# Kernel optimization log

Hardware: AMD Instinct MI355X
Metric: run time of the kernel (lower is better)

## Reference

```python
import jax, jax.numpy as jnp
import numpy as np

B, N, IN_DIM = 4, 2048, 128
HID, OUT_DIM, HEADS = 64, 64, 4
NEG = -1e9


def setup_inputs() -> dict:
    key = jax.random.key(0)
    ks = jax.random.split(key, 6)
    x = jax.random.normal(ks[0], (B, N, IN_DIM), dtype=jnp.float32)
    adj_matrix = jax.random.randint(ks[1], (B, N, N), 0, 2, dtype=jnp.int32)
    # per-head params: W [H, IN, HID], a [H, 2*HID] (Linear(2*HID,1) weight)
    W_heads = jax.random.normal(ks[2], (HEADS, IN_DIM, HID), dtype=jnp.float32) / np.sqrt(IN_DIM)
    a_heads = jax.random.normal(ks[3], (HEADS, 2 * HID), dtype=jnp.float32) / np.sqrt(2 * HID)
    W_out = jax.random.normal(ks[4], (HEADS * HID, OUT_DIM), dtype=jnp.float32) / np.sqrt(HEADS * HID)
    a_out = jax.random.normal(ks[5], (2 * OUT_DIM,), dtype=jnp.float32) / np.sqrt(2 * OUT_DIM)
    return {"x": x, "adj_matrix": adj_matrix, "W_heads": W_heads,
            "a_heads": a_heads, "W_out": W_out, "a_out": a_out}


def gat_layer(x, W, a, adj):
    # h: [B, N, D]
    h = jnp.einsum('bni,id->bnd', x, W)
    d = h.shape[-1]
    # a . [h_i ; h_j] = h_i . a1 + h_j . a2  (avoids N^2 concat materialization)
    s = h @ a[:d]          # [B, N] source term
    t = h @ a[d:]          # [B, N] target term
    e = s[:, :, None] + t[:, None, :]              # [B, N, N]
    e = jax.nn.leaky_relu(e, negative_slope=0.2)
    e = jnp.where(adj == 0, jnp.float32(NEG), e)
    alpha = jax.nn.softmax(e, axis=-1)             # dropout is identity in eval
    return jnp.einsum('bij,bjd->bid', alpha, h)


def reference(x, adj_matrix, W_heads, a_heads, W_out, a_out):
    # multi-head: vmap over head-stacked params -> [H, B, N, HID]
    heads = jax.vmap(gat_layer, in_axes=(None, 0, 0, None))(x, W_heads, a_heads, adj_matrix)
    # concat heads along feature dim: [B, N, H*HID]
    hcat = jnp.transpose(heads, (1, 2, 0, 3)).reshape(x.shape[0], x.shape[1], -1)
    return gat_layer(hcat, W_out, a_out, adj_matrix)
```

## Files before the change

kernel.cpp:

```cpp
#include <hip/hip_runtime.h>

#define B_ 4
#define N_ 2048
#define IND_ 128
#define NH_ 4

typedef short short8 __attribute__((ext_vector_type(8)));
typedef float float4v __attribute__((ext_vector_type(4)));

#if __has_builtin(__builtin_amdgcn_sbfe)
#define SBFE(x, o) __builtin_amdgcn_sbfe((int)(x), (unsigned)(o), 1u)
#else
#define SBFE(x, o) (((int)((unsigned)(x) << (31 - (o)))) >> 31)
#endif

typedef __attribute__((address_space(1))) const unsigned int as1_u32;
typedef __attribute__((address_space(3))) unsigned int as3_u32;
__device__ __forceinline__ void gl_lds16(const void* g, void* l) {
  __builtin_amdgcn_global_load_lds((as1_u32*)g, (as3_u32*)l, 16, 0, 0);
}

__device__ __forceinline__ unsigned int f2b_bits(float f) {
  unsigned int u = __float_as_uint(f);
  u += 0x7fffu + ((u >> 16) & 1u);
  return u >> 16;
}
__device__ __forceinline__ unsigned int pack_rne(float lo, float hi) {
  return f2b_bits(lo) | (f2b_bits(hi) << 16);
}
__device__ __forceinline__ unsigned int pack_trunc(float lo, float hi) {
  return __builtin_amdgcn_perm(__float_as_uint(hi), __float_as_uint(lo), 0x07060302u);
}
__device__ __forceinline__ float trunc_bf(float f) {
  return __uint_as_float(__float_as_uint(f) & 0xFFFF0000u);
}

union u4s8 { uint4 u; short8 s; };

__global__ __launch_bounds__(256) void gat_k0(
    const int* __restrict__ adj, unsigned long long* __restrict__ adjm,
    const float* __restrict__ Wh, const float* __restrict__ ah,
    const float* __restrict__ Wo, const float* __restrict__ ao,
    uint4* __restrict__ Wpk1, uint4* __restrict__ Wpk3,
    float* __restrict__ vsp1, float* __restrict__ vsp3) {
  const int bid = blockIdx.x;
  const int t = threadIdx.x;
  if (bid < B_ * N_ * N_ / 256) {
    const int gid = bid * 256 + t;
    const unsigned long long mval = __ballot(adj[gid] != 0);
    if ((t & 63) == 0) adjm[gid >> 6] = mval;
    return;
  }
  const int pb = bid - B_ * N_ * N_ / 256;
  if (pb < 32) {
    const int id = pb * 256 + t, e = id >> 6, l = id & 63;
    const int p = e & 1, ks = (e >> 1) & 3, dt = (e >> 3) & 3, h = e >> 5;
    const int d = dt * 16 + (l & 15), kb = ks * 32 + (l >> 4) * 8;
    unsigned u[4];
#pragma unroll
    for (int i = 0; i < 4; i++) {
      float w0 = Wh[(size_t)(h * IND_ + kb + 2 * i) * 64 + d];
      float w1 = Wh[(size_t)(h * IND_ + kb + 2 * i + 1) * 64 + d];
      if (p) {
        w0 -= __uint_as_float(f2b_bits(w0) << 16);
        w1 -= __uint_as_float(f2b_bits(w1) << 16);
      }
      u[i] = pack_rne(w0, w1);
    }
    Wpk1[e * 64 + l] = make_uint4(u[0], u[1], u[2], u[3]);
  } else if (pb < 48) {
    const int id = (pb - 32) * 256 + t, e = id >> 6, l = id & 63;
    const int p = e & 1, ks = (e >> 1) & 7, dt = e >> 4;
    const int d = dt * 16 + (l & 15), kb = ks * 32 + (l >> 4) * 8;
    unsigned u[4];
#pragma unroll
    for (int i = 0; i < 4; i++) {
      float w0 = Wo[(size_t)(kb + 2 * i) * 64 + d];
      float w1 = Wo[(size_t)(kb + 2 * i + 1) * 64 + d];
      if (p) {
        w0 -= __uint_as_float(f2b_bits(w0) << 16);
        w1 -= __uint_as_float(f2b_bits(w1) << 16);
      }
      u[i] = pack_rne(w0, w1);
    }
    Wpk3[e * 64 + l] = make_uint4(u[0], u[1], u[2], u[3]);
  } else if (pb < 52) {
    const int id = (pb - 48) * 256 + t;
    const int h = id >> 8, vec = (id >> 7) & 1, k = id & 127;
    const float* wr = Wh + (size_t)(h * IND_ + k) * 64;
    const float* av = ah + h * 128 + vec * 64;
    float s = 0.f;
#pragma unroll 8
    for (int d = 0; d < 64; d++) s = fmaf(wr[d], av[d], s);
    vsp1[(h * 2 + vec) * 128 + k] = s;
  } else {
    const int id = (pb - 52) * 256 + t;
    const int vec = id >> 8, k = id & 255;
    const float* wr = Wo + (size_t)k * 64;
    const float* av = ao + vec * 64;
    float s = 0.f;
#pragma unroll 8
    for (int d = 0; d < 64; d++) s = fmaf(wr[d], av[d], s);
    vsp3[vec * 256 + k] = s;
  }
}

__global__ __launch_bounds__(256) void gat_k1(
    const float* __restrict__ x, const uint4* __restrict__ Wpk1,
    const float* __restrict__ vsp1,
    unsigned short* __restrict__ h1T, float2* __restrict__ Es1, float2* __restrict__ Et1) {
  __shared__ float xf[16 * 132];
  __shared__ unsigned short xhi[16 * 136];
  __shared__ unsigned short xlo[16 * 136];
  const int b = blockIdx.y, j0 = blockIdx.x * 16;
  const int tid = threadIdx.x;
  const int jr = tid >> 4, k0 = (tid & 15) * 8;
  const float4* xg = (const float4*)(x + ((size_t)b * N_ + j0 + jr) * IND_ + k0);
  const float4 v0 = xg[0], v1 = xg[1];
  *(float4*)(xf + jr * 132 + k0) = v0;
  *(float4*)(xf + jr * 132 + k0 + 4) = v1;
  {
    unsigned hu[4], lu[4];
    hu[0] = pack_trunc(v0.x, v0.y); hu[1] = pack_trunc(v0.z, v0.w);
    hu[2] = pack_trunc(v1.x, v1.y); hu[3] = pack_trunc(v1.z, v1.w);
    lu[0] = pack_trunc(v0.x - trunc_bf(v0.x), v0.y - trunc_bf(v0.y));
    lu[1] = pack_trunc(v0.z - trunc_bf(v0.z), v0.w - trunc_bf(v0.w));
    lu[2] = pack_trunc(v1.x - trunc_bf(v1.x), v1.y - trunc_bf(v1.y));
    lu[3] = pack_trunc(v1.z - trunc_bf(v1.z), v1.w - trunc_bf(v1.w));
    *(uint4*)(xhi + jr * 136 + k0) = make_uint4(hu[0], hu[1], hu[2], hu[3]);
    *(uint4*)(xlo + jr * 136 + k0) = make_uint4(lu[0], lu[1], lu[2], lu[3]);
  }
  __syncthreads();
  const int h = tid >> 6, lane = tid & 63;
  const int m = lane & 15, q = lane >> 4;
  float4v acc[4] = {};
  const unsigned short* ap = xhi + m * 136 + q * 8;
  const unsigned short* alp = xlo + m * 136 + q * 8;
#pragma unroll
  for (int ks = 0; ks < 4; ks++) {
    const short8 ahi = *(const short8*)(ap + ks * 32);
    const short8 alo = *(const short8*)(alp + ks * 32);
#pragma unroll
    for (int dt = 0; dt < 4; dt++) {
      u4s8 bh, bl;
      bh.u = Wpk1[(((h * 4 + dt) * 4 + ks) * 2 + 0) * 64 + lane];
      bl.u = Wpk1[(((h * 4 + dt) * 4 + ks) * 2 + 1) * 64 + lane];
      acc[dt] = __builtin_amdgcn_mfma_f32_16x16x32_bf16(ahi, bh.s, acc[dt], 0, 0, 0);
      acc[dt] = __builtin_amdgcn_mfma_f32_16x16x32_bf16(alo, bh.s, acc[dt], 0, 0, 0);
      acc[dt] = __builtin_amdgcn_mfma_f32_16x16x32_bf16(ahi, bl.s, acc[dt], 0, 0, 0);
    }
  }
  const int hb = b * NH_ + h;
#pragma unroll
  for (int dt = 0; dt < 4; dt++) {
    const uint2 uu = make_uint2(pack_rne(acc[dt][0], acc[dt][1]),
                                pack_rne(acc[dt][2], acc[dt][3]));
    *(uint2*)(h1T + (size_t)(hb * 64 + dt * 16 + m) * N_ + j0 + q * 4) = uu;
  }
  const int vec = (tid >> 5) & 1, jd = (tid >> 1) & 15, half = tid & 1;
  const float* xr = xf + jd * 132 + half * 64;
  const float* vr = vsp1 + (h * 2 + vec) * 128 + half * 64;
  float dot = 0.f;
#pragma unroll
  for (int kk = 0; kk < 64; kk += 4) {
    const float4 xa = *(const float4*)(xr + kk);
    const float4 va = *(const float4*)(vr + kk);
    dot = fmaf(xa.x, va.x, dot); dot = fmaf(xa.y, va.y, dot);
    dot = fmaf(xa.z, va.z, dot); dot = fmaf(xa.w, va.w, dot);
  }
  dot += __shfl_xor(dot, 1);
  if (half == 0) {
    const float2 ev = make_float2(__expf(dot), __expf(0.2f * dot));
    if (vec == 0) Es1[(size_t)hb * N_ + j0 + jd] = ev;
    else          Et1[(size_t)hb * N_ + j0 + jd] = ev;
  }
}

__global__ __launch_bounds__(256) void gat_k2(
    const unsigned char* __restrict__ adjm, const unsigned short* __restrict__ h1T,
    const float2* __restrict__ Es1, const float2* __restrict__ Et1,
    float* __restrict__ hcat) {
  __shared__ float4 Ebuf[1024];
  __shared__ uint4 vbuf[2][256];
  const int b = blockIdx.z, h = blockIdx.y;
  const int tid = threadIdx.x;
  const int wv = tid >> 6, lane = tid & 63;
  const int m = lane & 15, q = lane >> 4;
  const int i0 = blockIdx.x * 64 + wv * 16;
  const int hb = b * NH_ + h;
  {
    const char* esrc = (const char*)(Et1 + (size_t)hb * N_);
    char* edst = (char*)Ebuf;
#pragma unroll
    for (int c = 0; c < 4; c++)
      gl_lds16(esrc + c * 4096 + tid * 16, edst + c * 4096 + tid * 16);
  }
  const char* vsrc = (const char*)(h1T + ((size_t)hb * 64 + (tid >> 2)) * N_) + (tid & 3) * 16;
  gl_lds16(vsrc, (char*)vbuf[0] + tid * 16);
  const float2 G = Es1[(size_t)hb * N_ + i0 + m];
  const float G1 = G.x, G2 = G.y;
  const float NSE = 1.0f / G1;
  const unsigned char* mrow = adjm + (size_t)(b * N_ + i0 + m) * (N_ / 8);
  const int q8 = q * 8;
  float4v acc[4] = {};
  float4v accS = {};
  const short8 ONES = {0x3F80, 0x3F80, 0x3F80, 0x3F80, 0x3F80, 0x3F80, 0x3F80, 0x3F80};
  uint4 mw = *(const uint4*)mrow;
  for (int it4 = 0; it4 < 16; it4++) {
#pragma unroll
    for (int s = 0; s < 4; s++) {
      const int it = it4 * 4 + s;
      __syncthreads();
      if (it + 1 < 64) gl_lds16(vsrc + (it + 1) * 64, (char*)vbuf[(it + 1) & 1] + tid * 16);
      const unsigned mword = s == 0 ? mw.x : s == 1 ? mw.y : s == 2 ? mw.z : mw.w;
      if (s == 3 && it4 < 15) mw = *(const uint4*)(mrow + (it4 + 1) * 16);
      const float4* ep = Ebuf + it * 16 + q * 4;
      unsigned pk[4];
#pragma unroll
      for (int p = 0; p < 4; p++) {
        const float4 e2 = ep[p];
        const bool c0 = e2.x >= NSE;
        const bool c1 = e2.z >= NSE;
        float w0 = (c0 ? G1 : G2) * (c0 ? e2.x : e2.y);
        float w1 = (c1 ? G1 : G2) * (c1 ? e2.z : e2.w);
        const int a0 = SBFE(mword, q8 + 2 * p);
        const int a1 = SBFE(mword, q8 + 2 * p + 1);
        pk[p] = pack_trunc(__uint_as_float(__float_as_uint(w0) & (unsigned)a0),
                           __uint_as_float(__float_as_uint(w1) & (unsigned)a1));
      }
      union { unsigned u[4]; short8 v; } cu;
      cu.u[0] = pk[0]; cu.u[1] = pk[1]; cu.u[2] = pk[2]; cu.u[3] = pk[3];
      const char* curv = (const char*)vbuf[it & 1];
#pragma unroll
      for (int dt = 0; dt < 4; dt++) {
        const short8 bf = *(const short8*)(curv + (dt * 16 + m) * 64 + q * 16);
        acc[dt] = __builtin_amdgcn_mfma_f32_16x16x32_bf16(cu.v, bf, acc[dt], 0, 0, 0);
      }
      accS = __builtin_amdgcn_mfma_f32_16x16x32_bf16(cu.v, ONES, accS, 0, 0, 0);
    }
  }
  float* ob = hcat + (size_t)b * N_ * 256 + h * 64 + m;
#pragma unroll
  for (int r = 0; r < 4; r++) {
    const float invS = 1.0f / accS[r];
    float* op = ob + (size_t)(i0 + q * 4 + r) * 256;
    op[0]  = acc[0][r] * invS;
    op[16] = acc[1][r] * invS;
    op[32] = acc[2][r] * invS;
    op[48] = acc[3][r] * invS;
  }
}

__global__ __launch_bounds__(256) void gat_k3(
    const float* __restrict__ hcat, const uint4* __restrict__ Wpk3,
    const float* __restrict__ vsp3,
    unsigned short* __restrict__ h2T, float2* __restrict__ Es2, float2* __restrict__ Et2) {
  __shared__ float xf[16 * 260];
  __shared__ unsigned short xhi[16 * 264];
  __shared__ unsigned short xlo[16 * 264];
  const int b = blockIdx.y, j0 = blockIdx.x * 16;
  const int tid = threadIdx.x;
  const int jr = tid >> 4, k0 = (tid & 15) * 16;
  const float4* xg = (const float4*)(hcat + ((size_t)b * N_ + j0 + jr) * 256 + k0);
  float4 v[4];
#pragma unroll
  for (int i = 0; i < 4; i++) v[i] = xg[i];
#pragma unroll
  for (int i = 0; i < 4; i++) *(float4*)(xf + jr * 260 + k0 + 4 * i) = v[i];
  {
    unsigned hu[8], lu[8];
#pragma unroll
    for (int i = 0; i < 4; i++) {
      hu[2 * i]     = pack_trunc(v[i].x, v[i].y);
      hu[2 * i + 1] = pack_trunc(v[i].z, v[i].w);
      lu[2 * i]     = pack_trunc(v[i].x - trunc_bf(v[i].x), v[i].y - trunc_bf(v[i].y));
      lu[2 * i + 1] = pack_trunc(v[i].z - trunc_bf(v[i].z), v[i].w - trunc_bf(v[i].w));
    }
    *(uint4*)(xhi + jr * 264 + k0)     = make_uint4(hu[0], hu[1], hu[2], hu[3]);
    *(uint4*)(xhi + jr * 264 + k0 + 8) = make_uint4(hu[4], hu[5], hu[6], hu[7]);
    *(uint4*)(xlo + jr * 264 + k0)     = make_uint4(lu[0], lu[1], lu[2], lu[3]);
    *(uint4*)(xlo + jr * 264 + k0 + 8) = make_uint4(lu[4], lu[5], lu[6], lu[7]);
  }
  __syncthreads();
  const int w = tid >> 6, lane = tid & 63;
  const int m = lane & 15, q = lane >> 4;
  float4v acc = {};
  const unsigned short* ap = xhi + m * 264 + q * 8;
  const unsigned short* alp = xlo + m * 264 + q * 8;
#pragma unroll
  for (int ks = 0; ks < 8; ks++) {
    const short8 ahi = *(const short8*)(ap + ks * 32);
    const short8 alo = *(const short8*)(alp + ks * 32);
    u4s8 bh, bl;
    bh.u = Wpk3[((w * 8 + ks) * 2 + 0) * 64 + lane];
    bl.u = Wpk3[((w * 8 + ks) * 2 + 1) * 64 + lane];
    acc = __builtin_amdgcn_mfma_f32_16x16x32_bf16(ahi, bh.s, acc, 0, 0, 0);
    acc = __builtin_amdgcn_mfma_f32_16x16x32_bf16(alo, bh.s, acc, 0, 0, 0);
    acc = __builtin_amdgcn_mfma_f32_16x16x32_bf16(ahi, bl.s, acc, 0, 0, 0);
  }
  {
    const uint2 uu = make_uint2(pack_rne(acc[0], acc[1]), pack_rne(acc[2], acc[3]));
    *(uint2*)(h2T + (size_t)(b * 64 + w * 16 + m) * N_ + j0 + q * 4) = uu;
  }
  const int vec = tid >> 7, jj = (tid >> 3) & 15, seg = tid & 7;
  const float* xr = xf + jj * 260 + seg * 4;
  const float* vr = vsp3 + vec * 256 + seg * 4;
  float dot = 0.f;
#pragma unroll
  for (int s = 0; s < 8; s++) {
    const float4 xa = *(const float4*)(xr + s * 32);
    const float4 va = *(const float4*)(vr + s * 32);
    dot = fmaf(xa.x, va.x, dot); dot = fmaf(xa.y, va.y, dot);
    dot = fmaf(xa.z, va.z, dot); dot = fmaf(xa.w, va.w, dot);
  }
  dot += __shfl_xor(dot, 1);
  dot += __shfl_xor(dot, 2);
  dot += __shfl_xor(dot, 4);
  if (seg == 0) {
    const float2 ev = make_float2(__expf(dot), __expf(0.2f * dot));
    if (vec == 0) Es2[(size_t)b * N_ + j0 + jj] = ev;
    else          Et2[(size_t)b * N_ + j0 + jj] = ev;
  }
}

__global__ __launch_bounds__(256) void gat_k4(
    const unsigned char* __restrict__ adjm, const unsigned short* __restrict__ h2T,
    const float2* __restrict__ Es2, const float2* __restrict__ Et2,
    float* __restrict__ p2, float* __restrict__ S2p) {
  __shared__ float4 Ebuf[256];
  __shared__ uint4 vbuf[2][256];
  const int b = blockIdx.z, js = blockIdx.y;
  const int tid = threadIdx.x;
  const int wv = tid >> 6, lane = tid & 63;
  const int m = lane & 15, q = lane >> 4;
  const int i0 = blockIdx.x * 64 + wv * 16;
  gl_lds16((const char*)(Et2 + (size_t)b * N_ + js * 512) + tid * 16,
           (char*)Ebuf + tid * 16);
  const char* vsrc = (const char*)(h2T + ((size_t)b * 64 + (tid >> 2)) * N_) +
                     (size_t)js * 1024 + (tid & 3) * 16;
  gl_lds16(vsrc, (char*)vbuf[0] + tid * 16);
  const float2 G = Es2[(size_t)b * N_ + i0 + m];
  const float G1 = G.x, G2 = G.y;
  const float NSE = 1.0f / G1;
  const unsigned char* mrow = adjm + (size_t)(b * N_ + i0 + m) * (N_ / 8) + js * 64;
  const int q8 = q * 8;
  float4v acc[4] = {};
  float4v accS = {};
  const short8 ONES = {0x3F80, 0x3F80, 0x3F80, 0x3F80, 0x3F80, 0x3F80, 0x3F80, 0x3F80};
  uint4 mw = *(const uint4*)mrow;
  for (int it4 = 0; it4 < 4; it4++) {
#pragma unroll
    for (int s = 0; s < 4; s++) {
      const int it = it4 * 4 + s;
      __syncthreads();
      if (it + 1 < 16) gl_lds16(vsrc + (it + 1) * 64, (char*)vbuf[(it + 1) & 1] + tid * 16);
      const unsigned mword = s == 0 ? mw.x : s == 1 ? mw.y : s == 2 ? mw.z : mw.w;
      if (s == 3 && it4 < 3) mw = *(const uint4*)(mrow + (it4 + 1) * 16);
      const float4* ep = Ebuf + it * 16 + q * 4;
      unsigned pk[4];
#pragma unroll
      for (int p = 0; p < 4; p++) {
        const float4 e2 = ep[p];
        const bool c0 = e2.x >= NSE;
        const bool c1 = e2.z >= NSE;
        float w0 = (c0 ? G1 : G2) * (c0 ? e2.x : e2.y);
        float w1 = (c1 ? G1 : G2) * (c1 ? e2.z : e2.w);
        const int a0 = SBFE(mword, q8 + 2 * p);
        const int a1 = SBFE(mword, q8 + 2 * p + 1);
        pk[p] = pack_trunc(__uint_as_float(__float_as_uint(w0) & (unsigned)a0),
                           __uint_as_float(__float_as_uint(w1) & (unsigned)a1));
      }
      union { unsigned u[4]; short8 v; } cu;
      cu.u[0] = pk[0]; cu.u[1] = pk[1]; cu.u[2] = pk[2]; cu.u[3] = pk[3];
      const char* curv = (const char*)vbuf[it & 1];
#pragma unroll
      for (int dt = 0; dt < 4; dt++) {
        const short8 bf = *(const short8*)(curv + (dt * 16 + m) * 64 + q * 16);
        acc[dt] = __builtin_amdgcn_mfma_f32_16x16x32_bf16(cu.v, bf, acc[dt], 0, 0, 0);
      }
      accS = __builtin_amdgcn_mfma_f32_16x16x32_bf16(cu.v, ONES, accS, 0, 0, 0);
    }
  }
  if (m == 0) {
#pragma unroll
    for (int r = 0; r < 4; r++)
      S2p[(size_t)(js * B_ + b) * N_ + i0 + q * 4 + r] = accS[r];
  }
  float* ob = p2 + (size_t)(js * B_ + b) * N_ * 64 + m;
#pragma unroll
  for (int r = 0; r < 4; r++) {
    float* op = ob + (size_t)(i0 + q * 4 + r) * 64;
    op[0]  = acc[0][r];
    op[16] = acc[1][r];
    op[32] = acc[2][r];
    op[48] = acc[3][r];
  }
}

__global__ __launch_bounds__(256) void gat_k5(
    const float* __restrict__ p2, const float* __restrict__ S2p, float* __restrict__ out) {
  const int gid = blockIdx.x * 256 + threadIdx.x;
  const int row = gid >> 4, c4 = gid & 15;
  float S = 0.f;
  float4 acc = make_float4(0.f, 0.f, 0.f, 0.f);
  const float4* pr = (const float4*)p2 + (size_t)row * 16 + c4;
#pragma unroll
  for (int s = 0; s < 4; s++) {
    S += S2p[(size_t)s * B_ * N_ + row];
    const float4 v = pr[(size_t)s * B_ * N_ * 16];
    acc.x += v.x; acc.y += v.y; acc.z += v.z; acc.w += v.w;
  }
  const float iv = 1.0f / S;
  acc.x *= iv; acc.y *= iv; acc.z *= iv; acc.w *= iv;
  ((float4*)out)[gid] = acc;
}

extern "C" void kernel_launch(void* const* d_in, const int* in_sizes, int n_in,
                              void* d_out, int out_size, void* d_ws, size_t ws_size,
                              hipStream_t stream) {
  (void)in_sizes; (void)n_in; (void)out_size; (void)ws_size;
  const float* x  = (const float*)d_in[0];
  const int* adj  = (const int*)d_in[1];
  const float* Wh = (const float*)d_in[2];
  const float* ah = (const float*)d_in[3];
  const float* Wo = (const float*)d_in[4];
  const float* ao = (const float*)d_in[5];
  float* out = (float*)d_out;

  char* base = (char*)d_ws;
  unsigned long long* adjm = (unsigned long long*)base;
  unsigned short* h1T = (unsigned short*)(base + 2097152);
  float2* Et1 = (float2*)(base + 6291456);
  float2* Es1 = (float2*)(base + 6553600);
  unsigned short* h2T = (unsigned short*)(base + 6815744);
  float2* Et2 = (float2*)(base + 7864320);
  float2* Es2 = (float2*)(base + 7929856);
  float* hcat = (float*)(base + 7995392);
  float* p2   = hcat;
  float* S2p  = (float*)(base + 16384000);
  uint4* Wpk1 = (uint4*)(base + 16512000);
  uint4* Wpk3 = (uint4*)(base + 16643072);
  float* vsp1 = (float*)(base + 16708608);
  float* vsp3 = (float*)(base + 16712704);

  gat_k0<<<dim3(B_ * N_ * N_ / 256 + 54), 256, 0, stream>>>(
      adj, adjm, Wh, ah, Wo, ao, Wpk1, Wpk3, vsp1, vsp3);
  gat_k1<<<dim3(N_ / 16, B_), 256, 0, stream>>>(x, Wpk1, vsp1, h1T, Es1, Et1);
  gat_k2<<<dim3(N_ / 64, NH_, B_), 256, 0, stream>>>(
      (const unsigned char*)adjm, h1T, Es1, Et1, hcat);
  gat_k3<<<dim3(N_ / 16, B_), 256, 0, stream>>>(hcat, Wpk3, vsp3, h2T, Es2, Et2);
  gat_k4<<<dim3(N_ / 64, 4, B_), 256, 0, stream>>>(
      (const unsigned char*)adjm, h2T, Es2, Et2, p2, S2p);
  gat_k5<<<dim3(B_ * N_ * 64 / 1024), 256, 0, stream>>>(p2, S2p, out);
}
```

Before: 178.0 us.

## Split layer-1 attention over key halves, widen K-steps, swizzle LDS value tiles

The layer-1 attention kernel now splits the neighbour dimension into two halves across extra blocks and writes unnormalized partial sums plus partial denominators. The next projection kernel merges and normalizes them. Both attention kernels move to 64-column chunks per sync, using an XOR-swizzled LDS layout for the value tile to avoid bank conflicts, and the layer-2 split grows from 4 to 8. Leaky-relu selection becomes a fmax instead of a threshold compare. The aim is more parallelism, fewer barriers and fewer bank conflicts, at the cost of extra partial-result traffic and a larger workspace.

```diff
diff --git a/kernel.cpp b/kernel.cpp
--- a/kernel.cpp
+++ b/kernel.cpp
@@ -176,95 +176,113 @@
   }
 }
 
-__global__ __launch_bounds__(256) void gat_k2(
+__global__ __launch_bounds__(256, 4) void gat_k2(
     const unsigned char* __restrict__ adjm, const unsigned short* __restrict__ h1T,
     const float2* __restrict__ Es1, const float2* __restrict__ Et1,
-    float* __restrict__ hcat) {
-  __shared__ float4 Ebuf[1024];
-  __shared__ uint4 vbuf[2][256];
-  const int b = blockIdx.z, h = blockIdx.y;
+    float* __restrict__ p1, float* __restrict__ S1p) {
+  __shared__ float4 Ebuf[512];
+  __shared__ uint4 vbuf[2][512];
+  const int b = blockIdx.z, h = blockIdx.y >> 1, js = blockIdx.y & 1;
   const int tid = threadIdx.x;
   const int wv = tid >> 6, lane = tid & 63;
   const int m = lane & 15, q = lane >> 4;
   const int i0 = blockIdx.x * 64 + wv * 16;
   const int hb = b * NH_ + h;
+  const int jbase = js * 1024;
   {
-    const char* esrc = (const char*)(Et1 + (size_t)hb * N_);
-    char* edst = (char*)Ebuf;
-#pragma unroll
-    for (int c = 0; c < 4; c++)
-      gl_lds16(esrc + c * 4096 + tid * 16, edst + c * 4096 + tid * 16);
-  }
-  const char* vsrc = (const char*)(h1T + ((size_t)hb * 64 + (tid >> 2)) * N_) + (tid & 3) * 16;
-  gl_lds16(vsrc, (char*)vbuf[0] + tid * 16);
+    const char* esrc = (const char*)(Et1 + (size_t)hb * N_ + jbase);
+    gl_lds16(esrc + tid * 16, (char*)Ebuf + tid * 16);
+    gl_lds16(esrc + 4096 + tid * 16, (char*)Ebuf + 4096 + tid * 16);
+  }
+  const int pg = (tid & 7) ^ ((tid >> 3) & 7);
+  const char* vsrc0 = (const char*)(h1T + ((size_t)hb * 64 + (tid >> 3)) * N_ + jbase) + pg * 16;
+  const char* vsrc1 = (const char*)(h1T + ((size_t)hb * 64 + 32 + (tid >> 3)) * N_ + jbase) + pg * 16;
+  gl_lds16(vsrc0, (char*)vbuf[0] + tid * 16);
+  gl_lds16(vsrc1, (char*)vbuf[0] + 4096 + tid * 16);
   const float2 G = Es1[(size_t)hb * N_ + i0 + m];
-  const float G1 = G.x, G2 = G.y;
-  const float NSE = 1.0f / G1;
-  const unsigned char* mrow = adjm + (size_t)(b * N_ + i0 + m) * (N_ / 8);
-  const int q8 = q * 8;
+  const unsigned char* mrow = adjm + (size_t)(b * N_ + i0 + m) * (N_ / 8) + js * 128;
   float4v acc[4] = {};
   float4v accS = {};
   const short8 ONES = {0x3F80, 0x3F80, 0x3F80, 0x3F80, 0x3F80, 0x3F80, 0x3F80, 0x3F80};
-  uint4 mw = *(const uint4*)mrow;
-  for (int it4 = 0; it4 < 16; it4++) {
-#pragma unroll
-    for (int s = 0; s < 4; s++) {
-      const int it = it4 * 4 + s;
-      __syncthreads();
-      if (it + 1 < 64) gl_lds16(vsrc + (it + 1) * 64, (char*)vbuf[(it + 1) & 1] + tid * 16);
-      const unsigned mword = s == 0 ? mw.x : s == 1 ? mw.y : s == 2 ? mw.z : mw.w;
-      if (s == 3 && it4 < 15) mw = *(const uint4*)(mrow + (it4 + 1) * 16);
-      const float4* ep = Ebuf + it * 16 + q * 4;
+  for (int it = 0; it < 16; it++) {
+    __syncthreads();
+    if (it + 1 < 16) {
+      gl_lds16(vsrc0 + (it + 1) * 128, (char*)vbuf[(it + 1) & 1] + tid * 16);
+      gl_lds16(vsrc1 + (it + 1) * 128, (char*)vbuf[(it + 1) & 1] + 4096 + tid * 16);
+    }
+    const uint2 mw2 = *(const uint2*)(mrow + it * 8);
+    const char* curv = (const char*)vbuf[it & 1];
+#pragma unroll
+    for (int c = 0; c < 2; c++) {
+      const unsigned mword = c ? mw2.y : mw2.x;
+      const float4* ep = Ebuf + it * 32 + c * 16 + q * 4;
       unsigned pk[4];
 #pragma unroll
       for (int p = 0; p < 4; p++) {
         const float4 e2 = ep[p];
-        const bool c0 = e2.x >= NSE;
-        const bool c1 = e2.z >= NSE;
-        float w0 = (c0 ? G1 : G2) * (c0 ? e2.x : e2.y);
-        float w1 = (c1 ? G1 : G2) * (c1 ? e2.z : e2.w);
-        const int a0 = SBFE(mword, q8 + 2 * p);
-        const int a1 = SBFE(mword, q8 + 2 * p + 1);
+        const float w0 = fmaxf(e2.x * G.x, e2.y * G.y);
+        const float w1 = fmaxf(e2.z * G.x, e2.w * G.y);
+        const int a0 = SBFE(mword, q * 8 + 2 * p);
+        const int a1 = SBFE(mword, q * 8 + 2 * p + 1);
         pk[p] = pack_trunc(__uint_as_float(__float_as_uint(w0) & (unsigned)a0),
                            __uint_as_float(__float_as_uint(w1) & (unsigned)a1));
       }
       union { unsigned u[4]; short8 v; } cu;
       cu.u[0] = pk[0]; cu.u[1] = pk[1]; cu.u[2] = pk[2]; cu.u[3] = pk[3];
-      const char* curv = (const char*)vbuf[it & 1];
 #pragma unroll
       for (int dt = 0; dt < 4; dt++) {
-        const short8 bf = *(const short8*)(curv + (dt * 16 + m) * 64 + q * 16);
+        const int d = dt * 16 + m;
+        const short8 bf =
+            *(const short8*)(curv + d * 128 + ((((c << 2) + q) ^ (m & 7)) << 4));
         acc[dt] = __builtin_amdgcn_mfma_f32_16x16x32_bf16(cu.v, bf, acc[dt], 0, 0, 0);
       }
       accS = __builtin_amdgcn_mfma_f32_16x16x32_bf16(cu.v, ONES, accS, 0, 0, 0);
     }
   }
-  float* ob = hcat + (size_t)b * N_ * 256 + h * 64 + m;
+  if (m == 0) {
+#pragma unroll
+    for (int r = 0; r < 4; r++)
+      S1p[((js * B_ + b) * NH_ + h) * N_ + i0 + q * 4 + r] = accS[r];
+  }
+  float* ob = p1 + (size_t)(js * B_ + b) * N_ * 256 + h * 64 + m;
 #pragma unroll
   for (int r = 0; r < 4; r++) {
-    const float invS = 1.0f / accS[r];
     float* op = ob + (size_t)(i0 + q * 4 + r) * 256;
-    op[0]  = acc[0][r] * invS;
-    op[16] = acc[1][r] * invS;
-    op[32] = acc[2][r] * invS;
-    op[48] = acc[3][r] * invS;
+    op[0]  = acc[0][r];
+    op[16] = acc[1][r];
+    op[32] = acc[2][r];
+    op[48] = acc[3][r];
   }
 }
 
 __global__ __launch_bounds__(256) void gat_k3(
-    const float* __restrict__ hcat, const uint4* __restrict__ Wpk3,
-    const float* __restrict__ vsp3,
+    const float* __restrict__ p1, const float* __restrict__ S1p,
+    const uint4* __restrict__ Wpk3, const float* __restrict__ vsp3,
     unsigned short* __restrict__ h2T, float2* __restrict__ Es2, float2* __restrict__ Et2) {
   __shared__ float xf[16 * 260];
   __shared__ unsigned short xhi[16 * 264];
   __shared__ unsigned short xlo[16 * 264];
+  __shared__ float sInv[16][4];
   const int b = blockIdx.y, j0 = blockIdx.x * 16;
   const int tid = threadIdx.x;
+  if (tid < 64) {
+    const int n = tid & 15, hh = tid >> 4;
+    const float Sv = S1p[((0 * B_ + b) * NH_ + hh) * N_ + j0 + n] +
+                     S1p[((1 * B_ + b) * NH_ + hh) * N_ + j0 + n];
+    sInv[n][hh] = 1.0f / Sv;
+  }
+  __syncthreads();
   const int jr = tid >> 4, k0 = (tid & 15) * 16;
-  const float4* xg = (const float4*)(hcat + ((size_t)b * N_ + j0 + jr) * 256 + k0);
+  const float4* g0 = (const float4*)(p1 + ((size_t)(0 * B_ + b) * N_ + j0 + jr) * 256 + k0);
+  const float4* g1 = (const float4*)(p1 + ((size_t)(1 * B_ + b) * N_ + j0 + jr) * 256 + k0);
+  const float iv = sInv[jr][k0 >> 6];
   float4 v[4];
 #pragma unroll
-  for (int i = 0; i < 4; i++) v[i] = xg[i];
+  for (int i = 0; i < 4; i++) {
+    const float4 a = g0[i], c = g1[i];
+    v[i].x = (a.x + c.x) * iv; v[i].y = (a.y + c.y) * iv;
+    v[i].z = (a.z + c.z) * iv; v[i].w = (a.w + c.w) * iv;
+  }
 #pragma unroll
   for (int i = 0; i < 4; i++) *(float4*)(xf + jr * 260 + k0 + 4 * i) = v[i];
   {
@@ -323,59 +341,61 @@
   }
 }
 
-__global__ __launch_bounds__(256) void gat_k4(
+__global__ __launch_bounds__(256, 4) void gat_k4(
     const unsigned char* __restrict__ adjm, const unsigned short* __restrict__ h2T,
     const float2* __restrict__ Es2, const float2* __restrict__ Et2,
     float* __restrict__ p2, float* __restrict__ S2p) {
-  __shared__ float4 Ebuf[256];
-  __shared__ uint4 vbuf[2][256];
+  __shared__ float4 Ebuf[128];
+  __shared__ uint4 vbuf[2][512];
   const int b = blockIdx.z, js = blockIdx.y;
   const int tid = threadIdx.x;
   const int wv = tid >> 6, lane = tid & 63;
   const int m = lane & 15, q = lane >> 4;
   const int i0 = blockIdx.x * 64 + wv * 16;
-  gl_lds16((const char*)(Et2 + (size_t)b * N_ + js * 512) + tid * 16,
-           (char*)Ebuf + tid * 16);
-  const char* vsrc = (const char*)(h2T + ((size_t)b * 64 + (tid >> 2)) * N_) +
-                     (size_t)js * 1024 + (tid & 3) * 16;
-  gl_lds16(vsrc, (char*)vbuf[0] + tid * 16);
+  const int jbase = js * 256;
+  if (tid < 128)
+    gl_lds16((const char*)(Et2 + (size_t)b * N_ + jbase) + tid * 16,
+             (char*)Ebuf + tid * 16);
+  const int pg = (tid & 7) ^ ((tid >> 3) & 7);
+  const char* vsrc0 = (const char*)(h2T + ((size_t)b * 64 + (tid >> 3)) * N_ + jbase) + pg * 16;
+  const char* vsrc1 = (const char*)(h2T + ((size_t)b * 64 + 32 + (tid >> 3)) * N_ + jbase) + pg * 16;
+  gl_lds16(vsrc0, (char*)vbuf[0] + tid * 16);
+  gl_lds16(vsrc1, (char*)vbuf[0] + 4096 + tid * 16);
   const float2 G = Es2[(size_t)b * N_ + i0 + m];
-  const float G1 = G.x, G2 = G.y;
-  const float NSE = 1.0f / G1;
-  const unsigned char* mrow = adjm + (size_t)(b * N_ + i0 + m) * (N_ / 8) + js * 64;
-  const int q8 = q * 8;
+  const unsigned char* mrow = adjm + (size_t)(b * N_ + i0 + m) * (N_ / 8) + js * 32;
   float4v acc[4] = {};
   float4v accS = {};
   const short8 ONES = {0x3F80, 0x3F80, 0x3F80, 0x3F80, 0x3F80, 0x3F80, 0x3F80, 0x3F80};
-  uint4 mw = *(const uint4*)mrow;
-  for (int it4 = 0; it4 < 4; it4++) {
-#pragma unroll
-    for (int s = 0; s < 4; s++) {
-      const int it = it4 * 4 + s;
-      __syncthreads();
-      if (it + 1 < 16) gl_lds16(vsrc + (it + 1) * 64, (char*)vbuf[(it + 1) & 1] + tid * 16);
-      const unsigned mword = s == 0 ? mw.x : s == 1 ? mw.y : s == 2 ? mw.z : mw.w;
-      if (s == 3 && it4 < 3) mw = *(const uint4*)(mrow + (it4 + 1) * 16);
-      const float4* ep = Ebuf + it * 16 + q * 4;
+  for (int it = 0; it < 4; it++) {
+    __syncthreads();
+    if (it + 1 < 4) {
+      gl_lds16(vsrc0 + (it + 1) * 128, (char*)vbuf[(it + 1) & 1] + tid * 16);
+      gl_lds16(vsrc1 + (it + 1) * 128, (char*)vbuf[(it + 1) & 1] + 4096 + tid * 16);
+    }
+    const uint2 mw2 = *(const uint2*)(mrow + it * 8);
+    const char* curv = (const char*)vbuf[it & 1];
+#pragma unroll
+    for (int c = 0; c < 2; c++) {
+      const unsigned mword = c ? mw2.y : mw2.x;
+      const float4* ep = Ebuf + it * 32 + c * 16 + q * 4;
       unsigned pk[4];
 #pragma unroll
       for (int p = 0; p < 4; p++) {
         const float4 e2 = ep[p];
-        const bool c0 = e2.x >= NSE;
-        const bool c1 = e2.z >= NSE;
-        float w0 = (c0 ? G1 : G2) * (c0 ? e2.x : e2.y);
-        float w1 = (c1 ? G1 : G2) * (c1 ? e2.z : e2.w);
-        const int a0 = SBFE(mword, q8 + 2 * p);
-        const int a1 = SBFE(mword, q8 + 2 * p + 1);
+        const float w0 = fmaxf(e2.x * G.x, e2.y * G.y);
+        const float w1 = fmaxf(e2.z * G.x, e2.w * G.y);
+        const int a0 = SBFE(mword, q * 8 + 2 * p);
+        const int a1 = SBFE(mword, q * 8 + 2 * p + 1);
         pk[p] = pack_trunc(__uint_as_float(__float_as_uint(w0) & (unsigned)a0),
                            __uint_as_float(__float_as_uint(w1) & (unsigned)a1));
       }
       union { unsigned u[4]; short8 v; } cu;
       cu.u[0] = pk[0]; cu.u[1] = pk[1]; cu.u[2] = pk[2]; cu.u[3] = pk[3];
-      const char* curv = (const char*)vbuf[it & 1];
 #pragma unroll
       for (int dt = 0; dt < 4; dt++) {
-        const short8 bf = *(const short8*)(curv + (dt * 16 + m) * 64 + q * 16);
+        const int d = dt * 16 + m;
+        const short8 bf =
+            *(const short8*)(curv + d * 128 + ((((c << 2) + q) ^ (m & 7)) << 4));
         acc[dt] = __builtin_amdgcn_mfma_f32_16x16x32_bf16(cu.v, bf, acc[dt], 0, 0, 0);
       }
       accS = __builtin_amdgcn_mfma_f32_16x16x32_bf16(cu.v, ONES, accS, 0, 0, 0);
@@ -405,7 +425,7 @@
   float4 acc = make_float4(0.f, 0.f, 0.f, 0.f);
   const float4* pr = (const float4*)p2 + (size_t)row * 16 + c4;
 #pragma unroll
-  for (int s = 0; s < 4; s++) {
+  for (int s = 0; s < 8; s++) {
     S += S2p[(size_t)s * B_ * N_ + row];
     const float4 v = pr[(size_t)s * B_ * N_ * 16];
     acc.x += v.x; acc.y += v.y; acc.z += v.z; acc.w += v.w;
@@ -429,27 +449,28 @@
 
   char* base = (char*)d_ws;
   unsigned long long* adjm = (unsigned long long*)base;
-  unsigned short* h1T = (unsigned short*)(base + 2097152);
-  float2* Et1 = (float2*)(base + 6291456);
-  float2* Es1 = (float2*)(base + 6553600);
-  unsigned short* h2T = (unsigned short*)(base + 6815744);
-  float2* Et2 = (float2*)(base + 7864320);
-  float2* Es2 = (float2*)(base + 7929856);
-  float* hcat = (float*)(base + 7995392);
-  float* p2   = hcat;
-  float* S2p  = (float*)(base + 16384000);
-  uint4* Wpk1 = (uint4*)(base + 16512000);
-  uint4* Wpk3 = (uint4*)(base + 16643072);
-  float* vsp1 = (float*)(base + 16708608);
-  float* vsp3 = (float*)(base + 16712704);
+  unsigned short* h1T = (unsigned short*)(base + 0x200000);
+  float2* Et1 = (float2*)(base + 0x600000);
+  float2* Es1 = (float2*)(base + 0x640000);
+  unsigned short* h2T = (unsigned short*)(base + 0x680000);
+  float2* Et2 = (float2*)(base + 0x780000);
+  float2* Es2 = (float2*)(base + 0x790000);
+  float* S1p  = (float*)(base + 0x7A0000);
+  float* S2p  = (float*)(base + 0x7E0000);
+  uint4* Wpk1 = (uint4*)(base + 0x820000);
+  uint4* Wpk3 = (uint4*)(base + 0x840000);
+  float* vsp1 = (float*)(base + 0x850000);
+  float* vsp3 = (float*)(base + 0x851000);
+  float* p1   = (float*)(base + 0x1000000);
+  float* p2   = p1;
 
   gat_k0<<<dim3(B_ * N_ * N_ / 256 + 54), 256, 0, stream>>>(
       adj, adjm, Wh, ah, Wo, ao, Wpk1, Wpk3, vsp1, vsp3);
   gat_k1<<<dim3(N_ / 16, B_), 256, 0, stream>>>(x, Wpk1, vsp1, h1T, Es1, Et1);
-  gat_k2<<<dim3(N_ / 64, NH_, B_), 256, 0, stream>>>(
-      (const unsigned char*)adjm, h1T, Es1, Et1, hcat);
-  gat_k3<<<dim3(N_ / 16, B_), 256, 0, stream>>>(hcat, Wpk3, vsp3, h2T, Es2, Et2);
-  gat_k4<<<dim3(N_ / 64, 4, B_), 256, 0, stream>>>(
+  gat_k2<<<dim3(N_ / 64, NH_ * 2, B_), 256, 0, stream>>>(
+      (const unsigned char*)adjm, h1T, Es1, Et1, p1, S1p);
+  gat_k3<<<dim3(N_ / 16, B_), 256, 0, stream>>>(p1, S1p, Wpk3, vsp3, h2T, Es2, Et2);
+  gat_k4<<<dim3(N_ / 64, 8, B_), 256, 0, stream>>>(
       (const unsigned char*)adjm, h2T, Es2, Et2, p2, S2p);
   gat_k5<<<dim3(B_ * N_ * 64 / 1024), 256, 0, stream>>>(p2, S2p, out);
 }
```

Result: faster. 169.3 us (-4.9%).

## Split key dimension across waves in attention kernels, reduce in LDS, drop k5

Applied to the files above, without the earlier changes.

The two attention-aggregation kernels now give each block 16 query rows and have the four waves each cover a quarter of the key range. Partial sums are combined through shared memory, which replaces the separate split-K reduction kernel gat_k5. Each wave streams its own V tiles with per-wave vmcnt waits instead of block-wide barriers, uses an XOR swizzle on the LDS layout to avoid bank conflicts, and computes the leaky-relu weight with fmaxf instead of a compare-and-select. The cost is more blocks, each re-reading the Et and V slices, and an extra LDS reduction step.

```diff
diff --git a/kernel.cpp b/kernel.cpp
--- a/kernel.cpp
+++ b/kernel.cpp
@@ -180,74 +180,93 @@
     const unsigned char* __restrict__ adjm, const unsigned short* __restrict__ h1T,
     const float2* __restrict__ Es1, const float2* __restrict__ Et1,
     float* __restrict__ hcat) {
-  __shared__ float4 Ebuf[1024];
-  __shared__ uint4 vbuf[2][256];
-  const int b = blockIdx.z, h = blockIdx.y;
+  __shared__ uint4 Ebuf[1024];
+  __shared__ uint4 vbuf[2][1024];
+  const int b = blockIdx.z, h = blockIdx.y, i0 = blockIdx.x * 16;
   const int tid = threadIdx.x;
   const int wv = tid >> 6, lane = tid & 63;
   const int m = lane & 15, q = lane >> 4;
-  const int i0 = blockIdx.x * 64 + wv * 16;
   const int hb = b * NH_ + h;
+  const int jb = wv * 512;
+  const uint4* mp = (const uint4*)(adjm + (size_t)(b * N_ + i0 + m) * (N_ / 8) + wv * 64);
+  const uint4 mk0 = mp[0], mk1 = mp[1], mk2 = mp[2], mk3 = mp[3];
+  const float2 G = Es1[(size_t)hb * N_ + i0 + m];
   {
-    const char* esrc = (const char*)(Et1 + (size_t)hb * N_);
-    char* edst = (char*)Ebuf;
-#pragma unroll
-    for (int c = 0; c < 4; c++)
-      gl_lds16(esrc + c * 4096 + tid * 16, edst + c * 4096 + tid * 16);
-  }
-  const char* vsrc = (const char*)(h1T + ((size_t)hb * 64 + (tid >> 2)) * N_) + (tid & 3) * 16;
-  gl_lds16(vsrc, (char*)vbuf[0] + tid * 16);
-  const float2 G = Es1[(size_t)hb * N_ + i0 + m];
-  const float G1 = G.x, G2 = G.y;
-  const float NSE = 1.0f / G1;
-  const unsigned char* mrow = adjm + (size_t)(b * N_ + i0 + m) * (N_ / 8);
-  const int q8 = q * 8;
+    const char* es = (const char*)(Et1 + (size_t)hb * N_ + jb);
+    char* ed = (char*)Ebuf + wv * 4096;
+#pragma unroll
+    for (int g = 0; g < 4; g++)
+      gl_lds16(es + g * 1024 + lane * 16, ed + g * 1024 + lane * 16);
+  }
+  const int vr = lane >> 2, vslot = lane & 3;
+  const unsigned short* vs_base =
+      h1T + ((size_t)hb * 64 + vr) * N_ + jb + (vslot ^ (vr & 3)) * 8;
+  char* ld_base = (char*)vbuf + wv * 4096 + lane * 16;
+#pragma unroll
+  for (int g = 0; g < 4; g++)
+    gl_lds16(vs_base + (size_t)g * 16 * N_, ld_base + g * 1024);
   float4v acc[4] = {};
   float4v accS = {};
   const short8 ONES = {0x3F80, 0x3F80, 0x3F80, 0x3F80, 0x3F80, 0x3F80, 0x3F80, 0x3F80};
-  uint4 mw = *(const uint4*)mrow;
-  for (int it4 = 0; it4 < 16; it4++) {
-#pragma unroll
-    for (int s = 0; s < 4; s++) {
-      const int it = it4 * 4 + s;
-      __syncthreads();
-      if (it + 1 < 64) gl_lds16(vsrc + (it + 1) * 64, (char*)vbuf[(it + 1) & 1] + tid * 16);
-      const unsigned mword = s == 0 ? mw.x : s == 1 ? mw.y : s == 2 ? mw.z : mw.w;
-      if (s == 3 && it4 < 15) mw = *(const uint4*)(mrow + (it4 + 1) * 16);
-      const float4* ep = Ebuf + it * 16 + q * 4;
-      unsigned pk[4];
-#pragma unroll
-      for (int p = 0; p < 4; p++) {
-        const float4 e2 = ep[p];
-        const bool c0 = e2.x >= NSE;
-        const bool c1 = e2.z >= NSE;
-        float w0 = (c0 ? G1 : G2) * (c0 ? e2.x : e2.y);
-        float w1 = (c1 ? G1 : G2) * (c1 ? e2.z : e2.w);
-        const int a0 = SBFE(mword, q8 + 2 * p);
-        const int a1 = SBFE(mword, q8 + 2 * p + 1);
-        pk[p] = pack_trunc(__uint_as_float(__float_as_uint(w0) & (unsigned)a0),
-                           __uint_as_float(__float_as_uint(w1) & (unsigned)a1));
-      }
-      union { unsigned u[4]; short8 v; } cu;
-      cu.u[0] = pk[0]; cu.u[1] = pk[1]; cu.u[2] = pk[2]; cu.u[3] = pk[3];
-      const char* curv = (const char*)vbuf[it & 1];
-#pragma unroll
-      for (int dt = 0; dt < 4; dt++) {
-        const short8 bf = *(const short8*)(curv + (dt * 16 + m) * 64 + q * 16);
-        acc[dt] = __builtin_amdgcn_mfma_f32_16x16x32_bf16(cu.v, bf, acc[dt], 0, 0, 0);
-      }
-      accS = __builtin_amdgcn_mfma_f32_16x16x32_bf16(cu.v, ONES, accS, 0, 0, 0);
-    }
-  }
-  float* ob = hcat + (size_t)b * N_ * 256 + h * 64 + m;
+#pragma unroll
+  for (int it = 0; it < 16; it++) {
+    if (it < 15) {
+#pragma unroll
+      for (int g = 0; g < 4; g++)
+        gl_lds16((const char*)(vs_base + (size_t)g * 16 * N_) + (it + 1) * 64,
+                 ld_base + (((it + 1) & 1) << 14) + g * 1024);
+      asm volatile("s_waitcnt vmcnt(4)" ::: "memory");
+    } else {
+      asm volatile("s_waitcnt vmcnt(0)" ::: "memory");
+    }
+    const uint4 mkk = (it >> 2) == 0 ? mk0 : (it >> 2) == 1 ? mk1 : (it >> 2) == 2 ? mk2 : mk3;
+    const unsigned mword =
+        (it & 3) == 0 ? mkk.x : (it & 3) == 1 ? mkk.y : (it & 3) == 2 ? mkk.z : mkk.w;
+    const float4* ep = (const float4*)((const char*)Ebuf + wv * 4096 + it * 256 + q * 64);
+    unsigned pk[4];
+#pragma unroll
+    for (int p = 0; p < 4; p++) {
+      const float4 e2 = ep[p];
+      const float w0 = fmaxf(e2.x * G.x, e2.y * G.y);
+      const float w1 = fmaxf(e2.z * G.x, e2.w * G.y);
+      const int a0 = SBFE(mword, q * 8 + 2 * p);
+      const int a1 = SBFE(mword, q * 8 + 2 * p + 1);
+      pk[p] = pack_trunc(__uint_as_float(__float_as_uint(w0) & (unsigned)a0),
+                         __uint_as_float(__float_as_uint(w1) & (unsigned)a1));
+    }
+    union { unsigned u[4]; short8 v; } cu;
+    cu.u[0] = pk[0]; cu.u[1] = pk[1]; cu.u[2] = pk[2]; cu.u[3] = pk[3];
+    const char* curv = (const char*)vbuf + ((it & 1) << 14) + wv * 4096;
+#pragma unroll
+    for (int dt = 0; dt < 4; dt++) {
+      const int row = dt * 16 + m;
+      const short8 bf = *(const short8*)(curv + row * 64 + ((q ^ (row & 3)) << 4));
+      acc[dt] = __builtin_amdgcn_mfma_f32_16x16x32_bf16(cu.v, bf, acc[dt], 0, 0, 0);
+    }
+    accS = __builtin_amdgcn_mfma_f32_16x16x32_bf16(cu.v, ONES, accS, 0, 0, 0);
+  }
+  __syncthreads();
+  float* red = (float*)vbuf;
+  float* redS = (float*)vbuf + 4096;
+#pragma unroll
+  for (int dt = 0; dt < 4; dt++)
+#pragma unroll
+    for (int r = 0; r < 4; r++)
+      red[wv * 1024 + (dt * 4 + r) * 64 + lane] = acc[dt][r];
+#pragma unroll
+  for (int r = 0; r < 4; r++)
+    redS[wv * 256 + r * 64 + lane] = accS[r];
+  __syncthreads();
+  float* ob = hcat + ((size_t)(b * N_ + i0)) * 256 + h * 64 + wv * 16 + m;
 #pragma unroll
   for (int r = 0; r < 4; r++) {
-    const float invS = 1.0f / accS[r];
-    float* op = ob + (size_t)(i0 + q * 4 + r) * 256;
-    op[0]  = acc[0][r] * invS;
-    op[16] = acc[1][r] * invS;
-    op[32] = acc[2][r] * invS;
-    op[48] = acc[3][r] * invS;
+    float v = 0.f, S = 0.f;
+#pragma unroll
+    for (int w2 = 0; w2 < 4; w2++) {
+      v += red[w2 * 1024 + (wv * 4 + r) * 64 + lane];
+      S += redS[w2 * 256 + r * 64 + lane];
+    }
+    ob[(size_t)(q * 4 + r) * 256] = v / S;
   }
 }
 
@@ -326,93 +345,94 @@
 __global__ __launch_bounds__(256) void gat_k4(
     const unsigned char* __restrict__ adjm, const unsigned short* __restrict__ h2T,
     const float2* __restrict__ Es2, const float2* __restrict__ Et2,
-    float* __restrict__ p2, float* __restrict__ S2p) {
-  __shared__ float4 Ebuf[256];
-  __shared__ uint4 vbuf[2][256];
-  const int b = blockIdx.z, js = blockIdx.y;
+    float* __restrict__ out) {
+  __shared__ uint4 Ebuf[1024];
+  __shared__ uint4 vbuf[2][1024];
+  const int b = blockIdx.y, i0 = blockIdx.x * 16;
   const int tid = threadIdx.x;
   const int wv = tid >> 6, lane = tid & 63;
   const int m = lane & 15, q = lane >> 4;
-  const int i0 = blockIdx.x * 64 + wv * 16;
-  gl_lds16((const char*)(Et2 + (size_t)b * N_ + js * 512) + tid * 16,
-           (char*)Ebuf + tid * 16);
-  const char* vsrc = (const char*)(h2T + ((size_t)b * 64 + (tid >> 2)) * N_) +
-                     (size_t)js * 1024 + (tid & 3) * 16;
-  gl_lds16(vsrc, (char*)vbuf[0] + tid * 16);
+  const int jb = wv * 512;
+  const uint4* mp = (const uint4*)(adjm + (size_t)(b * N_ + i0 + m) * (N_ / 8) + wv * 64);
+  const uint4 mk0 = mp[0], mk1 = mp[1], mk2 = mp[2], mk3 = mp[3];
   const float2 G = Es2[(size_t)b * N_ + i0 + m];
-  const float G1 = G.x, G2 = G.y;
-  const float NSE = 1.0f / G1;
-  const unsigned char* mrow = adjm + (size_t)(b * N_ + i0 + m) * (N_ / 8) + js * 64;
-  const int q8 = q * 8;
+  {
+    const char* es = (const char*)(Et2 + (size_t)b * N_ + jb);
+    char* ed = (char*)Ebuf + wv * 4096;
+#pragma unroll
+    for (int g = 0; g < 4; g++)
+      gl_lds16(es + g * 1024 + lane * 16, ed + g * 1024 + lane * 16);
+  }
+  const int vr = lane >> 2, vslot = lane & 3;
+  const unsigned short* vs_base =
+      h2T + ((size_t)b * 64 + vr) * N_ + jb + (vslot ^ (vr & 3)) * 8;
+  char* ld_base = (char*)vbuf + wv * 4096 + lane * 16;
+#pragma unroll
+  for (int g = 0; g < 4; g++)
+    gl_lds16(vs_base + (size_t)g * 16 * N_, ld_base + g * 1024);
   float4v acc[4] = {};
   float4v accS = {};
   const short8 ONES = {0x3F80, 0x3F80, 0x3F80, 0x3F80, 0x3F80, 0x3F80, 0x3F80, 0x3F80};
-  uint4 mw = *(const uint4*)mrow;
-  for (int it4 = 0; it4 < 4; it4++) {
-#pragma unroll
-    for (int s = 0; s < 4; s++) {
-      const int it = it4 * 4 + s;
-      __syncthreads();
-      if (it + 1 < 16) gl_lds16(vsrc + (it + 1) * 64, (char*)vbuf[(it + 1) & 1] + tid * 16);
-      const unsigned mword = s == 0 ? mw.x : s == 1 ? mw.y : s == 2 ? mw.z : mw.w;
-      if (s == 3 && it4 < 3) mw = *(const uint4*)(mrow + (it4 + 1) * 16);
-      const float4* ep = Ebuf + it * 16 + q * 4;
-      unsigned pk[4];
-#pragma unroll
-      for (int p = 0; p < 4; p++) {
-        const float4 e2 = ep[p];
-        const bool c0 = e2.x >= NSE;
-        const bool c1 = e2.z >= NSE;
-        float w0 = (c0 ? G1 : G2) * (c0 ? e2.x : e2.y);
-        float w1 = (c1 ? G1 : G2) * (c1 ? e2.z : e2.w);
-        const int a0 = SBFE(mword, q8 + 2 * p);
-        const int a1 = SBFE(mword, q8 + 2 * p + 1);
-        pk[p] = pack_trunc(__uint_as_float(__float_as_uint(w0) & (unsigned)a0),
-                           __uint_as_float(__float_as_uint(w1) & (unsigned)a1));
-      }
-      union { unsigned u[4]; short8 v; } cu;
-      cu.u[0] = pk[0]; cu.u[1] = pk[1]; cu.u[2] = pk[2]; cu.u[3] = pk[3];
-      const char* curv = (const char*)vbuf[it & 1];
-#pragma unroll
-      for (int dt = 0; dt < 4; dt++) {
-        const short8 bf = *(const short8*)(curv + (dt * 16 + m) * 64 + q * 16);
-        acc[dt] = __builtin_amdgcn_mfma_f32_16x16x32_bf16(cu.v, bf, acc[dt], 0, 0, 0);
-      }
-      accS = __builtin_amdgcn_mfma_f32_16x16x32_bf16(cu.v, ONES, accS, 0, 0, 0);
-    }
-  }
-  if (m == 0) {
+#pragma unroll
+  for (int it = 0; it < 16; it++) {
+    if (it < 15) {
+#pragma unroll
+      for (int g = 0; g < 4; g++)
+        gl_lds16((const char*)(vs_base + (size_t)g * 16 * N_) + (it + 1) * 64,
+                 ld_base + (((it + 1) & 1) << 14) + g * 1024);
+      asm volatile("s_waitcnt vmcnt(4)" ::: "memory");
+    } else {
+      asm volatile("s_waitcnt vmcnt(0)" ::: "memory");
+    }
+    const uint4 mkk = (it >> 2) == 0 ? mk0 : (it >> 2) == 1 ? mk1 : (it >> 2) == 2 ? mk2 : mk3;
+    const unsigned mword =
+        (it & 3) == 0 ? mkk.x : (it & 3) == 1 ? mkk.y : (it & 3) == 2 ? mkk.z : mkk.w;
+    const float4* ep = (const float4*)((const char*)Ebuf + wv * 4096 + it * 256 + q * 64);
+    unsigned pk[4];
+#pragma unroll
+    for (int p = 0; p < 4; p++) {
+      const float4 e2 = ep[p];
+      const float w0 = fmaxf(e2.x * G.x, e2.y * G.y);
+      const float w1 = fmaxf(e2.z * G.x, e2.w * G.y);
+      const int a0 = SBFE(mword, q * 8 + 2 * p);
+      const int a1 = SBFE(mword, q * 8 + 2 * p + 1);
+      pk[p] = pack_trunc(__uint_as_float(__float_as_uint(w0) & (unsigned)a0),
+                         __uint_as_float(__float_as_uint(w1) & (unsigned)a1));
+    }
+    union { unsigned u[4]; short8 v; } cu;
+    cu.u[0] = pk[0]; cu.u[1] = pk[1]; cu.u[2] = pk[2]; cu.u[3] = pk[3];
+    const char* curv = (const char*)vbuf + ((it & 1) << 14) + wv * 4096;
+#pragma unroll
+    for (int dt = 0; dt < 4; dt++) {
+      const int row = dt * 16 + m;
+      const short8 bf = *(const short8*)(curv + row * 64 + ((q ^ (row & 3)) << 4));
+      acc[dt] = __builtin_amdgcn_mfma_f32_16x16x32_bf16(cu.v, bf, acc[dt], 0, 0, 0);
+    }
+    accS = __builtin_amdgcn_mfma_f32_16x16x32_bf16(cu.v, ONES, accS, 0, 0, 0);
+  }
+  __syncthreads();
+  float* red = (float*)vbuf;
+  float* redS = (float*)vbuf + 4096;
+#pragma unroll
+  for (int dt = 0; dt < 4; dt++)
 #pragma unroll
     for (int r = 0; r < 4; r++)
-      S2p[(size_t)(js * B_ + b) * N_ + i0 + q * 4 + r] = accS[r];
-  }
-  float* ob = p2 + (size_t)(js * B_ + b) * N_ * 64 + m;
+      red[wv * 1024 + (dt * 4 + r) * 64 + lane] = acc[dt][r];
+#pragma unroll
+  for (int r = 0; r < 4; r++)
+    redS[wv * 256 + r * 64 + lane] = accS[r];
+  __syncthreads();
+  float* ob = out + ((size_t)(b * N_ + i0)) * 64 + wv * 16 + m;
 #pragma unroll
   for (int r = 0; r < 4; r++) {
-    float* op = ob + (size_t)(i0 + q * 4 + r) * 64;
-    op[0]  = acc[0][r];
-    op[16] = acc[1][r];
-    op[32] = acc[2][r];
-    op[48] = acc[3][r];
-  }
-}
-
-__global__ __launch_bounds__(256) void gat_k5(
-    const float* __restrict__ p2, const float* __restrict__ S2p, float* __restrict__ out) {
-  const int gid = blockIdx.x * 256 + threadIdx.x;
-  const int row = gid >> 4, c4 = gid & 15;
-  float S = 0.f;
-  float4 acc = make_float4(0.f, 0.f, 0.f, 0.f);
-  const float4* pr = (const float4*)p2 + (size_t)row * 16 + c4;
-#pragma unroll
-  for (int s = 0; s < 4; s++) {
-    S += S2p[(size_t)s * B_ * N_ + row];
-    const float4 v = pr[(size_t)s * B_ * N_ * 16];
-    acc.x += v.x; acc.y += v.y; acc.z += v.z; acc.w += v.w;
-  }
-  const float iv = 1.0f / S;
-  acc.x *= iv; acc.y *= iv; acc.z *= iv; acc.w *= iv;
-  ((float4*)out)[gid] = acc;
+    float v = 0.f, S = 0.f;
+#pragma unroll
+    for (int w2 = 0; w2 < 4; w2++) {
+      v += red[w2 * 1024 + (wv * 4 + r) * 64 + lane];
+      S += redS[w2 * 256 + r * 64 + lane];
+    }
+    ob[(size_t)(q * 4 + r) * 64] = v / S;
+  }
 }
 
 extern "C" void kernel_launch(void* const* d_in, const int* in_sizes, int n_in,
@@ -429,27 +449,24 @@
 
   char* base = (char*)d_ws;
   unsigned long long* adjm = (unsigned long long*)base;
-  unsigned short* h1T = (unsigned short*)(base + 2097152);
-  float2* Et1 = (float2*)(base + 6291456);
-  float2* Es1 = (float2*)(base + 6553600);
-  unsigned short* h2T = (unsigned short*)(base + 6815744);
-  float2* Et2 = (float2*)(base + 7864320);
-  float2* Es2 = (float2*)(base + 7929856);
-  float* hcat = (float*)(base + 7995392);
-  float* p2   = hcat;
-  float* S2p  = (float*)(base + 16384000);
-  uint4* Wpk1 = (uint4*)(base + 16512000);
-  uint4* Wpk3 = (uint4*)(base + 16643072);
-  float* vsp1 = (float*)(base + 16708608);
-  float* vsp3 = (float*)(base + 16712704);
+  unsigned short* h1T = (unsigned short*)(base + 0x200000);
+  float2* Et1 = (float2*)(base + 0x600000);
+  float2* Es1 = (float2*)(base + 0x640000);
+  unsigned short* h2T = (unsigned short*)(base + 0x680000);
+  float2* Et2 = (float2*)(base + 0x780000);
+  float2* Es2 = (float2*)(base + 0x790000);
+  uint4* Wpk1 = (uint4*)(base + 0x7A0000);
+  uint4* Wpk3 = (uint4*)(base + 0x7C0000);
+  float* vsp1 = (float*)(base + 0x7D0000);
+  float* vsp3 = (float*)(base + 0x7D1000);
+  float* hcat = (float*)(base + 0x800000);
 
   gat_k0<<<dim3(B_ * N_ * N_ / 256 + 54), 256, 0, stream>>>(
       adj, adjm, Wh, ah, Wo, ao, Wpk1, Wpk3, vsp1, vsp3);
   gat_k1<<<dim3(N_ / 16, B_), 256, 0, stream>>>(x, Wpk1, vsp1, h1T, Es1, Et1);
-  gat_k2<<<dim3(N_ / 64, NH_, B_), 256, 0, stream>>>(
+  gat_k2<<<dim3(N_ / 16, NH_, B_), 256, 0, stream>>>(
       (const unsigned char*)adjm, h1T, Es1, Et1, hcat);
   gat_k3<<<dim3(N_ / 16, B_), 256, 0, stream>>>(hcat, Wpk3, vsp3, h2T, Es2, Et2);
-  gat_k4<<<dim3(N_ / 64, 4, B_), 256, 0, stream>>>(
-      (const unsigned char*)adjm, h2T, Es2, Et2, p2, S2p);
-  gat_k5<<<dim3(B_ * N_ * 64 / 1024), 256, 0, stream>>>(p2, S2p, out);
-}
+  gat_k4<<<dim3(N_ / 16, B_), 256, 0, stream>>>(
+      (const unsigned char*)adjm, h2T, Es2, Et2, out);
+}
```

Measured after the change: 183.1 us. 1.03x slower.
